# Optimization experiments

Hardware: AMD Instinct MI355X
Metric: run time of the kernel (lower is better)

The kernel has to match this reference:

```python
import jax, jax.numpy as jnp
import numpy as np

HOPS = 3  # C[i].weight tied to A[i+1].weight -> HOPS+1 distinct tables E_0..E_HOPS


def setup_inputs() -> dict:
    key = jax.random.key(0)
    ks = jax.random.split(key, 10)
    B, M, K, E, G, V = 32, 2048, 4, 128, 128, 50000
    s = 1.0 / np.sqrt(E).astype(np.float32)
    context = jax.random.randint(ks[0], (B, M, K), 0, V)          # memory (triples)
    h_ = jax.random.normal(ks[1], (B, G), dtype=jnp.float32)      # prev GRU hidden
    y_ = jax.random.randint(ks[2], (B,), 0, V)                    # prev token
    emb = jax.random.normal(ks[3], (HOPS + 1, V, E), dtype=jnp.float32) * 0.1
    W_ih = jax.random.normal(ks[4], (3 * G, E), dtype=jnp.float32) * s
    W_hh = jax.random.normal(ks[5], (3 * G, G), dtype=jnp.float32) * s
    b_ih = jax.random.normal(ks[6], (3 * G,), dtype=jnp.float32) * s
    b_hh = jax.random.normal(ks[7], (3 * G,), dtype=jnp.float32) * s
    W_vocab = jax.random.normal(ks[8], (V, 2 * E), dtype=jnp.float32) * s
    b_vocab = jax.random.normal(ks[9], (V,), dtype=jnp.float32) * s
    return dict(context=context, h_=h_, y_=y_, emb=emb, W_ih=W_ih, W_hh=W_hh,
                b_ih=b_ih, b_hh=b_hh, W_vocab=W_vocab, b_vocab=b_vocab)


def gru_cell(x, h, W_ih, W_hh, b_ih, b_hh):
    # PyTorch GRU cell semantics (r, z, n gate order).
    gi = x @ W_ih.T + b_ih
    gh = h @ W_hh.T + b_hh
    i_r, i_z, i_n = jnp.split(gi, 3, axis=-1)
    h_r, h_z, h_n = jnp.split(gh, 3, axis=-1)
    r = jax.nn.sigmoid(i_r + h_r)
    z = jax.nn.sigmoid(i_z + h_z)
    n = jnp.tanh(i_n + r * h_n)
    return (1.0 - z) * n + z * h


def reference(context, h_, y_, emb, W_ih, W_hh, b_ih, b_hh, W_vocab, b_vocab):
    x = emb[0][y_]                                   # [B, E] A[0] embed of prev token
    h = gru_cell(x, h_, W_ih, W_hh, b_ih, b_hh)      # [B, G], G == E
    q = h
    o1 = None
    attn = None
    for hop in range(HOPS):
        mA = emb[hop][context].sum(axis=2)           # gather [B,M,K,E] -> sum over K -> [B,M,E]
        p = jnp.einsum('bme,be->bm', mA, q)          # attention scores over memory slots
        attn = jax.nn.softmax(p, axis=1)             # [B, M]
        mC = emb[hop + 1][context].sum(axis=2)       # C[hop] table (tied to A[hop+1])
        o = jnp.einsum('bm,bme->be', attn, mC)       # memory read [B, E]
        q = q + o
        if hop == 0:
            o1 = o
    logits = jnp.concatenate([h, o1], axis=1) @ W_vocab.T + b_vocab  # [B, V]
    p_vocab = jax.nn.softmax(logits, axis=1)
    return h, p_vocab, attn
```

## Files before the change

### kernel.cpp

```cpp
#include <hip/hip_runtime.h>
#include <math.h>

#define BB 32
#define MM 2048
#define KK 4
#define EE 128
#define GG 128
#define VV 50000
#define NT 391

__global__ __launch_bounds__(384) void gru_kernel(
    const float* __restrict__ emb0,
    const int*   __restrict__ y,
    const float* __restrict__ hprev,
    const float* __restrict__ W_ih,
    const float* __restrict__ W_hh,
    const float* __restrict__ b_ih,
    const float* __restrict__ b_hh,
    float* __restrict__ h_out,
    float* __restrict__ q,
    float* __restrict__ o1)
{
    int b = blockIdx.x;
    int t = threadIdx.x;
    __shared__ float x[EE], h[GG], gi[3*GG], gh[3*GG];
    if (t < EE)            x[t]       = emb0[(size_t)y[b]*EE + t];
    else if (t < 2*EE)     h[t-EE]    = hprev[b*GG + (t-EE)];
    if (t < EE) o1[b*EE + t] = 0.f;
    __syncthreads();
    {
        float accI = b_ih[t], accH = b_hh[t];
        const float* wi = W_ih + (size_t)t*EE;
        const float* wh = W_hh + (size_t)t*GG;
        #pragma unroll 8
        for (int e = 0; e < EE; e++) { accI += x[e]*wi[e]; accH += h[e]*wh[e]; }
        gi[t] = accI; gh[t] = accH;
    }
    __syncthreads();
    if (t < GG) {
        float r = 1.f/(1.f + __expf(-(gi[t]        + gh[t])));
        float z = 1.f/(1.f + __expf(-(gi[GG+t]     + gh[GG+t])));
        float n = tanhf(gi[2*GG+t] + r*gh[2*GG+t]);
        float hn = (1.f - z)*n + z*h[t];
        h_out[b*GG + t] = hn;
        q[b*GG + t]     = hn;
    }
}

__global__ __launch_bounds__(256) void t_kernel(
    const float* __restrict__ q,
    const float* __restrict__ embT,
    float* __restrict__ t)
{
    __shared__ float Ut[EE][32];
    __shared__ float Wt[32][132];
    int tid = threadIdx.x;
    for (int i = tid; i < EE*32; i += 256) {
        int e = i >> 5, b = i & 31;
        Ut[e][b] = q[b*EE + e];
    }
    int vg = tid & 31;
    int bg = tid >> 5;
    int v0 = blockIdx.x * 128;
    float acc[4][4];
    #pragma unroll
    for (int i = 0; i < 4; i++)
        #pragma unroll
        for (int j = 0; j < 4; j++) acc[i][j] = 0.f;

    int vrow = tid >> 1;
    int half = tid & 1;
    const float* wrow = embT + (size_t)(v0 + vrow)*EE + half*16;
    bool vok = (v0 + vrow) < VV;

    for (int ec = 0; ec < EE; ec += 32) {
        __syncthreads();
        #pragma unroll
        for (int j = 0; j < 4; j++) {
            float4 w = make_float4(0.f, 0.f, 0.f, 0.f);
            if (vok) w = *(const float4*)(wrow + ec + j*4);
            int e0 = half*16 + j*4;
            Wt[e0+0][vrow] = w.x;
            Wt[e0+1][vrow] = w.y;
            Wt[e0+2][vrow] = w.z;
            Wt[e0+3][vrow] = w.w;
        }
        __syncthreads();
        #pragma unroll 8
        for (int e = 0; e < 32; e++) {
            float4 w = *(const float4*)(&Wt[e][vg*4]);
            float4 u = *(const float4*)(&Ut[ec + e][bg*4]);
            acc[0][0] += w.x*u.x; acc[0][1] += w.x*u.y; acc[0][2] += w.x*u.z; acc[0][3] += w.x*u.w;
            acc[1][0] += w.y*u.x; acc[1][1] += w.y*u.y; acc[1][2] += w.y*u.z; acc[1][3] += w.y*u.w;
            acc[2][0] += w.z*u.x; acc[2][1] += w.z*u.y; acc[2][2] += w.z*u.z; acc[2][3] += w.z*u.w;
            acc[3][0] += w.w*u.x; acc[3][1] += w.w*u.y; acc[3][2] += w.w*u.z; acc[3][3] += w.w*u.w;
        }
    }
    #pragma unroll
    for (int i = 0; i < 4; i++) {
        int v = v0 + vg*4 + i;
        if (v < VV) {
            #pragma unroll
            for (int j = 0; j < 4; j++)
                t[(size_t)(bg*4 + j)*VV + v] = acc[i][j];
        }
    }
}

__global__ __launch_bounds__(256) void scores_lookup_kernel(
    const float* __restrict__ t,
    const int*   __restrict__ ctx,
    float* __restrict__ p)
{
    int gid = blockIdx.x*256 + threadIdx.x;
    int b   = gid >> 11;
    const int4 c = *(const int4*)(ctx + (size_t)gid*KK);
    const float* tb = t + (size_t)b*VV;
    p[gid] = tb[c.x] + tb[c.y] + tb[c.z] + tb[c.w];
}

template<int SAVE_O1>
__global__ __launch_bounds__(256) void oacc_fused_kernel(
    const float* __restrict__ embT,
    const int*   __restrict__ ctx,
    const float* __restrict__ p,
    float* __restrict__ S_out,
    float* __restrict__ q,
    float* __restrict__ o1)
{
    int blk = blockIdx.x;
    int b = blk >> 5, s = blk & 31;
    int t = threadIdx.x;
    int w = t >> 6, lane = t & 63;

    const float* row = p + (size_t)b*MM;
    float v[8];
    float mx = -INFINITY;
    #pragma unroll
    for (int i = 0; i < 8; i++) { v[i] = row[t + i*256]; mx = fmaxf(mx, v[i]); }
    __shared__ float red[6];
    #pragma unroll
    for (int off = 32; off; off >>= 1) mx = fmaxf(mx, __shfl_down(mx, off));
    if (lane == 0) red[w] = mx;
    __syncthreads();
    if (t == 0) red[4] = fmaxf(fmaxf(red[0],red[1]), fmaxf(red[2],red[3]));
    __syncthreads();
    mx = red[4];
    float sum = 0.f;
    #pragma unroll
    for (int i = 0; i < 8; i++) sum += __expf(v[i] - mx);
    #pragma unroll
    for (int off = 32; off; off >>= 1) sum += __shfl_down(sum, off);
    __syncthreads();
    if (lane == 0) red[w] = sum;
    __syncthreads();
    if (t == 0) red[5] = 1.f / (red[0]+red[1]+red[2]+red[3]);
    __syncthreads();
    float rs = red[5];

    int m0 = s*64 + w*16;
    float ax = 0.f, ay = 0.f;
    #pragma unroll 4
    for (int i = 0; i < 16; i++) {
        int m = m0 + i;
        float a = __expf(row[m] - mx) * rs;
        const int4 c = *(const int4*)(ctx + (size_t)(b*MM + m)*KK);
        float2 v0 = *(const float2*)(embT + (size_t)c.x*EE + lane*2);
        float2 v1 = *(const float2*)(embT + (size_t)c.y*EE + lane*2);
        float2 v2 = *(const float2*)(embT + (size_t)c.z*EE + lane*2);
        float2 v3 = *(const float2*)(embT + (size_t)c.w*EE + lane*2);
        float sx = v0.x + v1.x + v2.x + v3.x;
        float sy = v0.y + v1.y + v2.y + v3.y;
        *(float2*)(S_out + ((size_t)b*MM + m)*EE + lane*2) = make_float2(sx, sy);
        ax += a * sx;
        ay += a * sy;
    }
    __shared__ float acc_red[4][EE];
    acc_red[w][lane*2]   = ax;
    acc_red[w][lane*2+1] = ay;
    __syncthreads();
    if (t < EE) {
        float vv = acc_red[0][t] + acc_red[1][t] + acc_red[2][t] + acc_red[3][t];
        atomicAdd(&q[b*EE + t], vv);
        if (SAVE_O1) atomicAdd(&o1[b*EE + t], vv);
    }
}

__global__ __launch_bounds__(256) void scores_s_kernel(
    const float* __restrict__ S,
    const float* __restrict__ q,
    float* __restrict__ p)
{
    int gid  = blockIdx.x * 4 + (threadIdx.x >> 6);
    int lane = threadIdx.x & 63;
    int b    = gid >> 11;
    float2 sv = *(const float2*)(S + (size_t)gid*EE + lane*2);
    float2 qv = *(const float2*)(q + b*EE + lane*2);
    float acc = sv.x*qv.x + sv.y*qv.y;
    #pragma unroll
    for (int off = 32; off; off >>= 1) acc += __shfl_down(acc, off);
    if (lane == 0) p[gid] = acc;
}

__global__ __launch_bounds__(256) void softmax_m_kernel(
    const float* __restrict__ p,
    float* __restrict__ attn)
{
    int b = blockIdx.x, t = threadIdx.x;
    const float* row = p + (size_t)b*MM;
    float v[8];
    float mx = -INFINITY;
    #pragma unroll
    for (int i = 0; i < 8; i++) { v[i] = row[t + i*256]; mx = fmaxf(mx, v[i]); }
    __shared__ float red[6];
    int w = t >> 6, lane = t & 63;
    #pragma unroll
    for (int off = 32; off; off >>= 1) mx = fmaxf(mx, __shfl_down(mx, off));
    if (lane == 0) red[w] = mx;
    __syncthreads();
    if (t == 0) { float m2 = fmaxf(fmaxf(red[0],red[1]), fmaxf(red[2],red[3])); red[4] = m2; }
    __syncthreads();
    mx = red[4];
    float sum = 0.f;
    #pragma unroll
    for (int i = 0; i < 8; i++) { v[i] = __expf(v[i] - mx); sum += v[i]; }
    #pragma unroll
    for (int off = 32; off; off >>= 1) sum += __shfl_down(sum, off);
    if (lane == 0) red[w] = sum;
    __syncthreads();
    if (t == 0) { red[5] = 1.f / (red[0]+red[1]+red[2]+red[3]); }
    __syncthreads();
    float rs = red[5];
    #pragma unroll
    for (int i = 0; i < 8; i++) attn[(size_t)b*MM + t + i*256] = v[i]*rs;
}

__global__ __launch_bounds__(256) void logits_kernel(
    const float* __restrict__ h,
    const float* __restrict__ o1,
    const float* __restrict__ Wv,
    const float* __restrict__ bv,
    float* __restrict__ logits,
    float* __restrict__ part)
{
    __shared__ float Ut[256][32];
    __shared__ float Wt[32][132];
    int t = threadIdx.x;
    for (int i = t; i < 256*32; i += 256) {
        int e = i >> 5, b = i & 31;
        Ut[e][b] = (e < GG) ? h[b*GG + e] : o1[b*EE + (e - GG)];
    }
    int vg = t & 31;
    int bg = t >> 5;
    int v0 = blockIdx.x * 128;
    float acc[4][4];
    #pragma unroll
    for (int i = 0; i < 4; i++)
        #pragma unroll
        for (int j = 0; j < 4; j++) acc[i][j] = 0.f;

    int vrow = t >> 1;
    int half = t & 1;
    const float* wrow = Wv + (size_t)(v0 + vrow)*256 + half*16;
    bool vrok = (v0 + vrow) < VV;

    for (int ec = 0; ec < 256; ec += 32) {
        __syncthreads();
        #pragma unroll
        for (int j = 0; j < 4; j++) {
            float4 w = make_float4(0.f, 0.f, 0.f, 0.f);
            if (vrok) w = *(const float4*)(wrow + ec + j*4);
            int e0 = half*16 + j*4;
            Wt[e0+0][vrow] = w.x;
            Wt[e0+1][vrow] = w.y;
            Wt[e0+2][vrow] = w.z;
            Wt[e0+3][vrow] = w.w;
        }
        __syncthreads();
        #pragma unroll 8
        for (int e = 0; e < 32; e++) {
            float4 w = *(const float4*)(&Wt[e][vg*4]);
            float4 u = *(const float4*)(&Ut[ec + e][bg*4]);
            acc[0][0] += w.x*u.x; acc[0][1] += w.x*u.y; acc[0][2] += w.x*u.z; acc[0][3] += w.x*u.w;
            acc[1][0] += w.y*u.x; acc[1][1] += w.y*u.y; acc[1][2] += w.y*u.z; acc[1][3] += w.y*u.w;
            acc[2][0] += w.z*u.x; acc[2][1] += w.z*u.y; acc[2][2] += w.z*u.z; acc[2][3] += w.z*u.w;
            acc[3][0] += w.w*u.x; acc[3][1] += w.w*u.y; acc[3][2] += w.w*u.z; acc[3][3] += w.w*u.w;
        }
    }
    #pragma unroll
    for (int i = 0; i < 4; i++) {
        int v = v0 + vg*4 + i;
        bool ok = v < VV;
        float bb = ok ? bv[v] : 0.f;
        #pragma unroll
        for (int j = 0; j < 4; j++) {
            float val = ok ? (acc[i][j] + bb) : -INFINITY;
            acc[i][j] = val;
            if (ok) logits[(size_t)(bg*4 + j)*VV + v] = val;
        }
    }
    #pragma unroll
    for (int j = 0; j < 4; j++) {
        float m = fmaxf(fmaxf(acc[0][j], acc[1][j]), fmaxf(acc[2][j], acc[3][j]));
        #pragma unroll
        for (int off = 16; off; off >>= 1) m = fmaxf(m, __shfl_down(m, off, 32));
        m = __shfl(m, 0, 32);
        float s = 0.f;
        #pragma unroll
        for (int i = 0; i < 4; i++) s += __expf(acc[i][j] - m);
        #pragma unroll
        for (int off = 16; off; off >>= 1) s += __shfl_down(s, off, 32);
        if (vg == 0) {
            int b = bg*4 + j;
            part[((size_t)b*NT + blockIdx.x)*2]     = m;
            part[((size_t)b*NT + blockIdx.x)*2 + 1] = s;
        }
    }
}

__global__ __launch_bounds__(256) void vfinal_kernel(
    float* __restrict__ logits,
    const float* __restrict__ part)
{
    int i0  = blockIdx.x*256;
    int tid = threadIdx.x;
    int b0  = i0 / VV;
    int last = min(i0 + 255, BB*VV - 1);
    int bL  = last / VV;
    __shared__ float redm[256], reds[256];
    __shared__ float statM[2], statR[2];
    for (int pass = 0; pass < 2; pass++) {
        int b = b0 + pass;
        if (b > bL) break;
        float m = -INFINITY, s = 0.f;
        for (int tt = tid; tt < NT; tt += 256) {
            float pm = part[((size_t)b*NT + tt)*2];
            float ps = part[((size_t)b*NT + tt)*2 + 1];
            float M2 = fmaxf(m, pm);
            s = s*__expf(m - M2) + ps*__expf(pm - M2);
            m = M2;
        }
        redm[tid] = m; reds[tid] = s;
        __syncthreads();
        for (int off = 128; off; off >>= 1) {
            if (tid < off) {
                float m2 = redm[tid+off], s2 = reds[tid+off];
                float M2 = fmaxf(redm[tid], m2);
                reds[tid] = reds[tid]*__expf(redm[tid]-M2) + s2*__expf(m2-M2);
                redm[tid] = M2;
            }
            __syncthreads();
        }
        if (tid == 0) { statM[pass] = redm[0]; statR[pass] = 1.f / reds[0]; }
        __syncthreads();
    }
    int i = i0 + tid;
    if (i < BB*VV) {
        int b = i / VV;
        int pass = b - b0;
        logits[i] = __expf(logits[i] - statM[pass]) * statR[pass];
    }
}

extern "C" void kernel_launch(void* const* d_in, const int* in_sizes, int n_in,
                              void* d_out, int out_size, void* d_ws, size_t ws_size,
                              hipStream_t stream) {
    const int*   ctx    = (const int*)  d_in[0];
    const float* h_prev = (const float*)d_in[1];
    const int*   y      = (const int*)  d_in[2];
    const float* emb    = (const float*)d_in[3];
    const float* W_ih   = (const float*)d_in[4];
    const float* W_hh   = (const float*)d_in[5];
    const float* b_ih   = (const float*)d_in[6];
    const float* b_hh   = (const float*)d_in[7];
    const float* Wv     = (const float*)d_in[8];
    const float* bv     = (const float*)d_in[9];

    float* out_h    = (float*)d_out;
    float* out_pv   = out_h + BB*GG;
    float* out_attn = out_pv + (size_t)BB*VV;

    float* ws   = (float*)d_ws;
    float* q    = ws;
    float* o1   = q + BB*EE;
    float* p    = o1 + BB*EE;
    float* tbuf = p + BB*MM;
    float* S1   = tbuf + (size_t)BB*VV;
    float* S2   = S1 + (size_t)BB*MM*EE;
    float* part = S2 + (size_t)BB*MM*EE;

    const float* e0 = emb;
    const float* e1 = emb + (size_t)1*VV*EE;
    const float* e2 = emb + (size_t)2*VV*EE;

    gru_kernel<<<BB, 384, 0, stream>>>(emb, y, h_prev, W_ih, W_hh, b_ih, b_hh, out_h, q, o1);

    t_kernel<<<NT, 256, 0, stream>>>(q, e0, tbuf);
    scores_lookup_kernel<<<(BB*MM)/256, 256, 0, stream>>>(tbuf, ctx, p);
    oacc_fused_kernel<1><<<BB*32, 256, 0, stream>>>(e1, ctx, p, S1, q, o1);

    scores_s_kernel<<<(BB*MM)/4, 256, 0, stream>>>(S1, q, p);
    oacc_fused_kernel<0><<<BB*32, 256, 0, stream>>>(e2, ctx, p, S2, q, nullptr);

    scores_s_kernel<<<(BB*MM)/4, 256, 0, stream>>>(S2, q, p);
    softmax_m_kernel<<<BB, 256, 0, stream>>>(p, out_attn);

    logits_kernel<<<NT, 256, 0, stream>>>(out_h, o1, Wv, bv, out_pv, part);
    vfinal_kernel<<<(BB*VV + 255)/256, 256, 0, stream>>>(out_pv, part);
}
```

Before: 316.7 us.

## Merge score kernels with independent vocab logits/normalize work via block-index split

The hop-2 scores kernel and the vocab logits GEMM are merged into one launch, with blocks below SBLK computing scores and the rest computing logits tiles. The hop-3 scores kernel is likewise merged with the vocab softmax finalize. The logits depend only on h and o1, which are ready after hop 1, so this overlaps independent work and removes two launches. In exchange, the scores-path blocks now carry the large shared-memory footprint of the logits path, which may lower occupancy for those many small blocks.

After: 330.5 us. +4.3%, slower.

```diff
diff --git a/kernel.cpp b/kernel.cpp
--- a/kernel.cpp
+++ b/kernel.cpp
@@ -8,6 +8,8 @@
 #define GG 128
 #define VV 50000
 #define NT 391
+#define SBLK 16384
+#define VFB 6250
 
 __global__ __launch_bounds__(384) void gru_kernel(
     const float* __restrict__ emb0,
@@ -186,22 +188,6 @@
     }
 }
 
-__global__ __launch_bounds__(256) void scores_s_kernel(
-    const float* __restrict__ S,
-    const float* __restrict__ q,
-    float* __restrict__ p)
-{
-    int gid  = blockIdx.x * 4 + (threadIdx.x >> 6);
-    int lane = threadIdx.x & 63;
-    int b    = gid >> 11;
-    float2 sv = *(const float2*)(S + (size_t)gid*EE + lane*2);
-    float2 qv = *(const float2*)(q + b*EE + lane*2);
-    float acc = sv.x*qv.x + sv.y*qv.y;
-    #pragma unroll
-    for (int off = 32; off; off >>= 1) acc += __shfl_down(acc, off);
-    if (lane == 0) p[gid] = acc;
-}
-
 __global__ __launch_bounds__(256) void softmax_m_kernel(
     const float* __restrict__ p,
     float* __restrict__ attn)
@@ -235,7 +221,10 @@
     for (int i = 0; i < 8; i++) attn[(size_t)b*MM + t + i*256] = v[i]*rs;
 }
 
-__global__ __launch_bounds__(256) void logits_kernel(
+__global__ __launch_bounds__(256) void sl_kernel(
+    const float* __restrict__ S,
+    const float* __restrict__ q,
+    float* __restrict__ p,
     const float* __restrict__ h,
     const float* __restrict__ o1,
     const float* __restrict__ Wv,
@@ -245,22 +234,35 @@
 {
     __shared__ float Ut[256][32];
     __shared__ float Wt[32][132];
-    int t = threadIdx.x;
-    for (int i = t; i < 256*32; i += 256) {
+    int tid = threadIdx.x;
+    if (blockIdx.x < SBLK) {
+        int gid  = blockIdx.x * 4 + (tid >> 6);
+        int lane = tid & 63;
+        int b    = gid >> 11;
+        float2 sv = *(const float2*)(S + (size_t)gid*EE + lane*2);
+        float2 qv = *(const float2*)(q + b*EE + lane*2);
+        float acc = sv.x*qv.x + sv.y*qv.y;
+        #pragma unroll
+        for (int off = 32; off; off >>= 1) acc += __shfl_down(acc, off);
+        if (lane == 0) p[gid] = acc;
+        return;
+    }
+    int tile = blockIdx.x - SBLK;
+    for (int i = tid; i < 256*32; i += 256) {
         int e = i >> 5, b = i & 31;
         Ut[e][b] = (e < GG) ? h[b*GG + e] : o1[b*EE + (e - GG)];
     }
-    int vg = t & 31;
-    int bg = t >> 5;
-    int v0 = blockIdx.x * 128;
+    int vg = tid & 31;
+    int bg = tid >> 5;
+    int v0 = tile * 128;
     float acc[4][4];
     #pragma unroll
     for (int i = 0; i < 4; i++)
         #pragma unroll
         for (int j = 0; j < 4; j++) acc[i][j] = 0.f;
 
-    int vrow = t >> 1;
-    int half = t & 1;
+    int vrow = tid >> 1;
+    int half = tid & 1;
     const float* wrow = Wv + (size_t)(v0 + vrow)*256 + half*16;
     bool vrok = (v0 + vrow) < VV;
 
@@ -312,23 +314,38 @@
         for (int off = 16; off; off >>= 1) s += __shfl_down(s, off, 32);
         if (vg == 0) {
             int b = bg*4 + j;
-            part[((size_t)b*NT + blockIdx.x)*2]     = m;
-            part[((size_t)b*NT + blockIdx.x)*2 + 1] = s;
-        }
-    }
-}
-
-__global__ __launch_bounds__(256) void vfinal_kernel(
+            part[((size_t)b*NT + tile)*2]     = m;
+            part[((size_t)b*NT + tile)*2 + 1] = s;
+        }
+    }
+}
+
+__global__ __launch_bounds__(256) void sv_kernel(
+    const float* __restrict__ S,
+    const float* __restrict__ q,
+    float* __restrict__ p,
     float* __restrict__ logits,
     const float* __restrict__ part)
 {
-    int i0  = blockIdx.x*256;
     int tid = threadIdx.x;
+    __shared__ float redm[256], reds[256];
+    __shared__ float statM[2], statR[2];
+    if (blockIdx.x < SBLK) {
+        int gid  = blockIdx.x * 4 + (tid >> 6);
+        int lane = tid & 63;
+        int b    = gid >> 11;
+        float2 sv = *(const float2*)(S + (size_t)gid*EE + lane*2);
+        float2 qv = *(const float2*)(q + b*EE + lane*2);
+        float acc = sv.x*qv.x + sv.y*qv.y;
+        #pragma unroll
+        for (int off = 32; off; off >>= 1) acc += __shfl_down(acc, off);
+        if (lane == 0) p[gid] = acc;
+        return;
+    }
+    int i0  = (blockIdx.x - SBLK)*256;
     int b0  = i0 / VV;
     int last = min(i0 + 255, BB*VV - 1);
     int bL  = last / VV;
-    __shared__ float redm[256], reds[256];
-    __shared__ float statM[2], statR[2];
     for (int pass = 0; pass < 2; pass++) {
         int b = b0 + pass;
         if (b > bL) break;
@@ -397,14 +414,14 @@
 
     t_kernel<<<NT, 256, 0, stream>>>(q, e0, tbuf);
     scores_lookup_kernel<<<(BB*MM)/256, 256, 0, stream>>>(tbuf, ctx, p);
+
     oacc_fused_kernel<1><<<BB*32, 256, 0, stream>>>(e1, ctx, p, S1, q, o1);
 
-    scores_s_kernel<<<(BB*MM)/4, 256, 0, stream>>>(S1, q, p);
+    sl_kernel<<<SBLK + NT, 256, 0, stream>>>(S1, q, p, out_h, o1, Wv, bv, out_pv, part);
+
     oacc_fused_kernel<0><<<BB*32, 256, 0, stream>>>(e2, ctx, p, S2, q, nullptr);
 
-    scores_s_kernel<<<(BB*MM)/4, 256, 0, stream>>>(S2, q, p);
+    sv_kernel<<<SBLK + VFB, 256, 0, stream>>>(S2, q, p, out_pv, part);
+
     softmax_m_kernel<<<BB, 256, 0, stream>>>(p, out_attn);
-
-    logits_kernel<<<NT, 256, 0, stream>>>(out_h, o1, Wv, bv, out_pv, part);
-    vfinal_kernel<<<(BB*VV + 255)/256, 256, 0, stream>>>(out_pv, part);
-}
+}
```
